# Optimization experiments

Hardware: AMD Instinct MI355X
Metric: run time of the kernel (lower is better)

Reference implementation:

```python
import jax, jax.numpy as jnp
import numpy as np

UNITS = 512
MODELS = 64
BATCH = 64
INPUT_DIM = 512


def setup_inputs() -> dict:
    key = jax.random.key(0)
    ks = jax.random.split(key, 6)
    scale = 0.05  # keep gates in a sane range like 'random_normal' init
    return {
        "inputs": jax.random.normal(ks[0], (MODELS, BATCH, INPUT_DIM), jnp.float32),
        "h_tm1": jax.random.normal(ks[1], (MODELS, BATCH, UNITS), jnp.float32),
        "c_tm1": jax.random.normal(ks[2], (MODELS, BATCH, UNITS), jnp.float32),
        "kernel": jax.random.normal(ks[3], (MODELS, INPUT_DIM, 4 * UNITS), jnp.float32) * scale,
        "recurrent_kernel": jax.random.normal(ks[4], (MODELS, UNITS, 4 * UNITS), jnp.float32) * scale,
        "bias": jax.random.normal(ks[5], (MODELS, 1, 4 * UNITS), jnp.float32) * scale,
    }


def reference(inputs, h_tm1, c_tm1, kernel, recurrent_kernel, bias):
    # batched over the models axis: [m,b,d] @ [m,d,4u] -> [m,b,4u]
    z = jnp.einsum('mbd,mdu->mbu', inputs, kernel)
    z = z + jnp.einsum('mbh,mhu->mbu', h_tm1, recurrent_kernel)
    z = z + bias  # broadcasts over batch
    z0, z1, z2, z3 = jnp.split(z, 4, axis=-1)
    i = jax.nn.sigmoid(z0)
    f = jax.nn.sigmoid(z1)
    c = f * c_tm1 + i * jnp.tanh(z2)
    o = jax.nn.sigmoid(z3)
    h = o * jnp.tanh(c)
    return (h, h, c)
```

## Files before the change

kernel.cpp:

```cpp
#include <hip/hip_runtime.h>
#include <hip/hip_bf16.h>

#define MODELS 64
#define BATCH 64
#define IN_DIM 512
#define UNITS 512
#define NCOLS 2048
#define GRAN_PER_TENSOR (MODELS * 16 * 4 * 64)

typedef __attribute__((ext_vector_type(8))) short short8;
typedef __attribute__((ext_vector_type(4))) float f32x4;

static __device__ __forceinline__ short f2bf(float f) {
    return __builtin_bit_cast(short, __float2bfloat16(f));
}
static __device__ __forceinline__ float sigmoidf_(float x) {
    return 1.0f / (1.0f + __expf(-x));
}
static __device__ __forceinline__ float tanhf_(float x) {
    float e = __expf(-2.0f * fabsf(x));
    float r = (1.0f - e) / (1.0f + e);
    return copysignf(r, x);
}

__global__ __launch_bounds__(256) void prepack_A_kernel(
    const float* __restrict__ x, const float* __restrict__ h,
    short8* __restrict__ P)
{
    const int t = blockIdx.x * 256 + threadIdx.x;
    const int tensor = t >> 18;
    const int r = t & (GRAN_PER_TENSOR - 1);
    const int kg = r & 3;
    const int row = (r >> 2) & 63;
    const int ks = (r >> 8) & 15;
    const int m = r >> 12;
    const float* src = (tensor ? h : x) + ((size_t)(m * 64 + row) * 512 + ks * 32 + kg * 8);
    f32x4 a0 = *(const f32x4*)src;
    f32x4 a1 = *(const f32x4*)(src + 4);
    short8 v;
    v[0] = f2bf(a0[0]); v[1] = f2bf(a0[1]); v[2] = f2bf(a0[2]); v[3] = f2bf(a0[3]);
    v[4] = f2bf(a1[0]); v[5] = f2bf(a1[1]); v[6] = f2bf(a1[2]); v[7] = f2bf(a1[3]);
    P[(size_t)tensor * GRAN_PER_TENSOR + (size_t)((m * 16 + ks) * 4 + kg) * 64 + row] = v;
}

__global__ __launch_bounds__(512, 4) void lstm_main_kernel(
    const float* __restrict__ c_tm1,
    const float* __restrict__ kernel_,
    const float* __restrict__ rkernel,
    const float* __restrict__ bias,
    const short8* __restrict__ Pa,
    float* __restrict__ out)
{
    __shared__ float lds[16384];

    const int bid = blockIdx.x;
    const int m = bid >> 3;
    const int u0 = (bid & 7) * 64;
    const int tid = threadIdx.x;
    const int wave = tid >> 6;
    const int lane = tid & 63;
    const int col16 = lane & 15;
    const int kq = lane >> 4;

    const int wcol = kq * 512 + u0 + col16 * 4;

    const float* wbase[2] = { kernel_ + (size_t)m * IN_DIM * NCOLS,
                              rkernel + (size_t)m * UNITS * NCOLS };
    const short8* pabase[2] = { Pa + (size_t)m * 4096,
                                Pa + GRAN_PER_TENSOR + (size_t)m * 4096 };

    f32x4 acc[4][2];
#pragma unroll
    for (int bt = 0; bt < 4; ++bt)
#pragma unroll
        for (int c = 0; c < 2; ++c) acc[bt][c] = (f32x4){0.f, 0.f, 0.f, 0.f};

    auto STAGE = [&](int step, int bufsel) {
        const float* wb = wbase[step >> 4];
        const int krow0 = (step & 15) * 32;
#pragma unroll
        for (int j = 0; j < 4; ++j) {
            const int k = j * 8 + wave;
            const float* src = wb + (size_t)(krow0 + k) * NCOLS + wcol;
            float* dst = lds + bufsel * 8192 + k * 256;
            __builtin_amdgcn_global_load_lds(
                (const __attribute__((address_space(1))) void*)src,
                (__attribute__((address_space(3))) void*)dst, 16, 0, 0);
        }
    };

    STAGE(0, 0);

    short8 af[4];
    for (int t = 0; t < 32; ++t) {
        const int cur = t & 1;
        {
            const short8* pb = pabase[t >> 4] + (size_t)((t & 15) * 4 + kq) * 64 + col16;
#pragma unroll
            for (int bt = 0; bt < 4; ++bt) {
                asm volatile("global_load_dwordx4 %0, %1, off"
                             : "=v"(af[bt]) : "v"(pb + bt * 16) : "memory");
            }
        }
        if (t < 31) {
            STAGE(t + 1, cur ^ 1);
            asm volatile("s_waitcnt vmcnt(4)"
                         : "+v"(af[0]), "+v"(af[1]), "+v"(af[2]), "+v"(af[3]) :: "memory");
        } else {
            asm volatile("s_waitcnt vmcnt(0)"
                         : "+v"(af[0]), "+v"(af[1]), "+v"(af[2]), "+v"(af[3]) :: "memory");
        }
        asm volatile("s_barrier" ::: "memory");

        {
            const float* lb = lds + cur * 8192;
#pragma unroll
            for (int c = 0; c < 2; ++c) {
                const int cb = (wave * 2 + c) * 16 + col16;
                short8 bfr;
#pragma unroll
                for (int i = 0; i < 8; ++i)
                    bfr[i] = f2bf(lb[(kq * 8 + i) * 256 + cb]);
#pragma unroll
                for (int bt = 0; bt < 4; ++bt)
                    acc[bt][c] = __builtin_amdgcn_mfma_f32_16x16x32_bf16(
                        af[bt], bfr, acc[bt][c], 0, 0, 0);
            }
        }
        asm volatile("s_waitcnt lgkmcnt(0)" ::: "memory");
        asm volatile("s_barrier" ::: "memory");
    }

#pragma unroll
    for (int bt = 0; bt < 4; ++bt)
#pragma unroll
        for (int c = 0; c < 2; ++c)
#pragma unroll
            for (int r = 0; r < 4; ++r)
                lds[(size_t)(bt * 16 + kq * 4 + r) * 256 + (wave * 2 + c) * 16 + col16] =
                    acc[bt][c][r];
    __syncthreads();

    const int b = tid >> 3;
    const int ug = (tid & 7) * 8;

    float zi[8], zf[8], zc[8], zo[8];
    *(f32x4*)&zi[0] = *(const f32x4*)&lds[b * 256 + 0 + ug];
    *(f32x4*)&zi[4] = *(const f32x4*)&lds[b * 256 + 0 + ug + 4];
    *(f32x4*)&zf[0] = *(const f32x4*)&lds[b * 256 + 64 + ug];
    *(f32x4*)&zf[4] = *(const f32x4*)&lds[b * 256 + 64 + ug + 4];
    *(f32x4*)&zc[0] = *(const f32x4*)&lds[b * 256 + 128 + ug];
    *(f32x4*)&zc[4] = *(const f32x4*)&lds[b * 256 + 128 + ug + 4];
    *(f32x4*)&zo[0] = *(const f32x4*)&lds[b * 256 + 192 + ug];
    *(f32x4*)&zo[4] = *(const f32x4*)&lds[b * 256 + 192 + ug + 4];

    const float* bb = bias + (size_t)m * NCOLS;
    float bi[8], bf_[8], bc[8], bo[8];
    *(f32x4*)&bi[0] = *(const f32x4*)&bb[0 * 512 + u0 + ug];
    *(f32x4*)&bi[4] = *(const f32x4*)&bb[0 * 512 + u0 + ug + 4];
    *(f32x4*)&bf_[0] = *(const f32x4*)&bb[1 * 512 + u0 + ug];
    *(f32x4*)&bf_[4] = *(const f32x4*)&bb[1 * 512 + u0 + ug + 4];
    *(f32x4*)&bc[0] = *(const f32x4*)&bb[2 * 512 + u0 + ug];
    *(f32x4*)&bc[4] = *(const f32x4*)&bb[2 * 512 + u0 + ug + 4];
    *(f32x4*)&bo[0] = *(const f32x4*)&bb[3 * 512 + u0 + ug];
    *(f32x4*)&bo[4] = *(const f32x4*)&bb[3 * 512 + u0 + ug + 4];

    const size_t cidx = (size_t)m * (BATCH * UNITS) + (size_t)b * UNITS + u0 + ug;
    float cp[8];
    *(f32x4*)&cp[0] = *(const f32x4*)&c_tm1[cidx];
    *(f32x4*)&cp[4] = *(const f32x4*)&c_tm1[cidx + 4];

    float hv[8], cv[8];
#pragma unroll
    for (int j = 0; j < 8; ++j) {
        const float ig = sigmoidf_(zi[j] + bi[j]);
        const float fg = sigmoidf_(zf[j] + bf_[j]);
        const float cand = tanhf_(zc[j] + bc[j]);
        const float og = sigmoidf_(zo[j] + bo[j]);
        const float c = fg * cp[j] + ig * cand;
        cv[j] = c;
        hv[j] = og * tanhf_(c);
    }

    float* hout0 = out;
    float* hout1 = out + (size_t)MODELS * BATCH * UNITS;
    float* cout = out + 2 * (size_t)MODELS * BATCH * UNITS;
    *(f32x4*)&hout0[cidx] = *(const f32x4*)&hv[0];
    *(f32x4*)&hout0[cidx + 4] = *(const f32x4*)&hv[4];
    *(f32x4*)&hout1[cidx] = *(const f32x4*)&hv[0];
    *(f32x4*)&hout1[cidx + 4] = *(const f32x4*)&hv[4];
    *(f32x4*)&cout[cidx] = *(const f32x4*)&cv[0];
    *(f32x4*)&cout[cidx + 4] = *(const f32x4*)&cv[4];
}

extern "C" void kernel_launch(void* const* d_in, const int* in_sizes, int n_in,
                              void* d_out, int out_size, void* d_ws, size_t ws_size,
                              hipStream_t stream) {
    const float* inputs = (const float*)d_in[0];
    const float* h_tm1 = (const float*)d_in[1];
    const float* c_tm1 = (const float*)d_in[2];
    const float* kernel_ = (const float*)d_in[3];
    const float* rkernel = (const float*)d_in[4];
    const float* bias = (const float*)d_in[5];
    float* out = (float*)d_out;

    short8* P = (short8*)d_ws;
    hipLaunchKernelGGL(prepack_A_kernel, dim3(2 * GRAN_PER_TENSOR / 256), dim3(256),
                       0, stream, inputs, h_tm1, P);
    hipLaunchKernelGGL(lstm_main_kernel, dim3(MODELS * 8), dim3(512), 0, stream,
                       c_tm1, kernel_, rkernel, bias, P, out);
}
```

Before: 135.2 us.

## Swizzle LDS weight tile and prefetch A fragments one step ahead

The weight rows written into LDS by the direct-to-LDS loads are now XOR-swizzled by row group, and the reader applies the matching XOR. This removes the bank conflicts that came from the four k-quads reading rows with a 256-float stride. The main loop is also unrolled by two with separate A-fragment registers, so each step's A loads are issued one step earlier and overlap the previous MFMA compute. The cost is more VGPRs for the second A buffer and more outstanding memory operations, which could lower occupancy.

New measurement: 136.6 us. No clear change (+1.1%).

```diff
diff --git a/kernel.cpp b/kernel.cpp
--- a/kernel.cpp
+++ b/kernel.cpp
@@ -62,8 +62,6 @@
     const int col16 = lane & 15;
     const int kq = lane >> 4;
 
-    const int wcol = kq * 512 + u0 + col16 * 4;
-
     const float* wbase[2] = { kernel_ + (size_t)m * IN_DIM * NCOLS,
                               rkernel + (size_t)m * UNITS * NCOLS };
     const short8* pabase[2] = { Pa + (size_t)m * 4096,
@@ -81,52 +79,63 @@
 #pragma unroll
         for (int j = 0; j < 4; ++j) {
             const int k = j * 8 + wave;
-            const float* src = wb + (size_t)(krow0 + k) * NCOLS + wcol;
+            const float* src = wb + (size_t)(krow0 + k) * NCOLS
+                             + kq * 512 + u0 + ((col16 ^ (j << 1)) * 4);
             float* dst = lds + bufsel * 8192 + k * 256;
             __builtin_amdgcn_global_load_lds(
                 (const __attribute__((address_space(1))) void*)src,
                 (__attribute__((address_space(3))) void*)dst, 16, 0, 0);
         }
     };
-
+    auto LOADA = [&](int step, short8* af) {
+        const short8* pb = pabase[step >> 4] + (size_t)((step & 15) * 4 + kq) * 64 + col16;
+#pragma unroll
+        for (int bt = 0; bt < 4; ++bt)
+            asm volatile("global_load_dwordx4 %0, %1, off"
+                         : "=v"(af[bt]) : "v"(pb + bt * 16) : "memory");
+    };
+    auto COMPUTE = [&](int bufsel, short8* af) {
+        const float* lb = lds + bufsel * 8192;
+#pragma unroll
+        for (int c = 0; c < 2; ++c) {
+            const int cb = (wave * 2 + c) * 16 + col16;
+            const int cbs = cb ^ (kq << 3);
+            short8 bfr;
+#pragma unroll
+            for (int i = 0; i < 8; ++i)
+                bfr[i] = f2bf(lb[(kq * 8 + i) * 256 + cbs]);
+#pragma unroll
+            for (int bt = 0; bt < 4; ++bt)
+                acc[bt][c] = __builtin_amdgcn_mfma_f32_16x16x32_bf16(
+                    af[bt], bfr, acc[bt][c], 0, 0, 0);
+        }
+    };
+
+    short8 afA[4], afB[4];
     STAGE(0, 0);
-
-    short8 af[4];
-    for (int t = 0; t < 32; ++t) {
-        const int cur = t & 1;
-        {
-            const short8* pb = pabase[t >> 4] + (size_t)((t & 15) * 4 + kq) * 64 + col16;
-#pragma unroll
-            for (int bt = 0; bt < 4; ++bt) {
-                asm volatile("global_load_dwordx4 %0, %1, off"
-                             : "=v"(af[bt]) : "v"(pb + bt * 16) : "memory");
-            }
-        }
-        if (t < 31) {
-            STAGE(t + 1, cur ^ 1);
-            asm volatile("s_waitcnt vmcnt(4)"
-                         : "+v"(af[0]), "+v"(af[1]), "+v"(af[2]), "+v"(af[3]) :: "memory");
+    LOADA(0, afA);
+
+    for (int tp = 0; tp < 16; ++tp) {
+        const int te = 2 * tp;
+        STAGE(te + 1, 1);
+        LOADA(te + 1, afB);
+        asm volatile("s_waitcnt vmcnt(8)"
+                     : "+v"(afA[0]), "+v"(afA[1]), "+v"(afA[2]), "+v"(afA[3]) :: "memory");
+        asm volatile("s_barrier" ::: "memory");
+        COMPUTE(0, afA);
+        asm volatile("s_waitcnt lgkmcnt(0)" ::: "memory");
+        asm volatile("s_barrier" ::: "memory");
+        if (tp < 15) {
+            STAGE(te + 2, 0);
+            LOADA(te + 2, afA);
+            asm volatile("s_waitcnt vmcnt(8)"
+                         : "+v"(afB[0]), "+v"(afB[1]), "+v"(afB[2]), "+v"(afB[3]) :: "memory");
         } else {
             asm volatile("s_waitcnt vmcnt(0)"
-                         : "+v"(af[0]), "+v"(af[1]), "+v"(af[2]), "+v"(af[3]) :: "memory");
+                         : "+v"(afB[0]), "+v"(afB[1]), "+v"(afB[2]), "+v"(afB[3]) :: "memory");
         }
         asm volatile("s_barrier" ::: "memory");
-
-        {
-            const float* lb = lds + cur * 8192;
-#pragma unroll
-            for (int c = 0; c < 2; ++c) {
-                const int cb = (wave * 2 + c) * 16 + col16;
-                short8 bfr;
-#pragma unroll
-                for (int i = 0; i < 8; ++i)
-                    bfr[i] = f2bf(lb[(kq * 8 + i) * 256 + cb]);
-#pragma unroll
-                for (int bt = 0; bt < 4; ++bt)
-                    acc[bt][c] = __builtin_amdgcn_mfma_f32_16x16x32_bf16(
-                        af[bt], bfr, acc[bt][c], 0, 0, 0);
-            }
-        }
+        COMPUTE(1, afB);
         asm volatile("s_waitcnt lgkmcnt(0)" ::: "memory");
         asm volatile("s_barrier" ::: "memory");
     }
```
